# Performance work log

Measured on AMD Instinct MI355X. Metric: run time of the kernel, lower is better.

The kernel has to match this reference:

```python
import jax, jax.numpy as jnp
import numpy as np

D_MODEL = 1024
N_HEADS = 16
D_K = D_MODEL // N_HEADS
RANK = 16
LORA_SCALING = 32.0 / RANK  # alpha / rank = 2.0
LN_EPS = 1e-5


def _lora_linear(x, w, b, A, B):
    # torch nn.Linear: x @ w.T + b ; LoRA: (x @ A @ B) * scaling
    return x @ w.T + b + (x @ A @ B) * LORA_SCALING


def setup_inputs() -> dict:
    key = jax.random.key(0)
    ks = jax.random.split(key, 20)
    d = {}
    d['x'] = jax.random.normal(ks[0], (4, 1024, D_MODEL), dtype=jnp.float32)
    i = 1
    for p in ('q', 'k', 'v', 'o'):
        d[f'{p}_w'] = jax.random.normal(ks[i], (D_MODEL, D_MODEL), dtype=jnp.float32) * (1.0 / np.sqrt(D_MODEL)); i += 1
        d[f'{p}_b'] = jax.random.normal(ks[i], (D_MODEL,), dtype=jnp.float32) * 0.01; i += 1
        d[f'{p}_A'] = jax.random.normal(ks[i], (D_MODEL, RANK), dtype=jnp.float32) * 0.01; i += 1
        d[f'{p}_B'] = jax.random.normal(ks[i], (RANK, D_MODEL), dtype=jnp.float32) * 0.01; i += 1
    d['ln_g'] = jnp.ones((D_MODEL,), dtype=jnp.float32)
    d['ln_b'] = jnp.zeros((D_MODEL,), dtype=jnp.float32)
    return d


def reference(x, q_w, q_b, q_A, q_B, k_w, k_b, k_A, k_B,
              v_w, v_b, v_A, v_B, o_w, o_b, o_A, o_B, ln_g, ln_b):
    B, S, _ = x.shape
    # QKV projections with LoRA, reshape to [B, H, S, d_k]
    def split_heads(t):
        return t.reshape(B, S, N_HEADS, D_K).transpose(0, 2, 1, 3)
    Q = split_heads(_lora_linear(x, q_w, q_b, q_A, q_B))
    K = split_heads(_lora_linear(x, k_w, k_b, k_A, k_B))
    V = split_heads(_lora_linear(x, v_w, v_b, v_A, v_B))

    scores = jnp.einsum('bhqd,bhkd->bhqk', Q, K) / jnp.sqrt(jnp.float32(D_K))
    attn = jax.nn.softmax(scores, axis=-1)  # dropout is identity in eval
    ctx = jnp.einsum('bhqk,bhkd->bhqd', attn, V)
    ctx = ctx.transpose(0, 2, 1, 3).reshape(B, S, D_MODEL)

    out = _lora_linear(ctx, o_w, o_b, o_A, o_B)
    # residual + LayerNorm
    h = out + x
    mu = jnp.mean(h, axis=-1, keepdims=True)
    var = jnp.mean(jnp.square(h - mu), axis=-1, keepdims=True)
    normed = (h - mu) * jax.lax.rsqrt(var + LN_EPS) * ln_g + ln_b
    return normed, attn.mean(axis=1)
```

## Files before the change

kernel.cpp:

```cpp
#include <hip/hip_runtime.h>

#define DMODEL 1024
#define NHEADS 16
#define DHEAD  64
#define RANK   16
#define BATCH  4
#define SEQ    1024
#define MTOT   (BATCH*SEQ)
#define QSCALE 0.18033688011112042f

typedef __bf16 bf16;
typedef __bf16 bf16x8 __attribute__((ext_vector_type(8)));
typedef __bf16 bf16x4 __attribute__((ext_vector_type(4)));
typedef float  f32x4  __attribute__((ext_vector_type(4)));
typedef float  f32x16 __attribute__((ext_vector_type(16)));

__device__ __forceinline__ int swz128(int row, int byte_in_row) {
  int slot = byte_in_row >> 4;
  return row * 128 + (((slot ^ (row & 7)) << 4) | (byte_in_row & 15));
}

__device__ __forceinline__ void gll16(const void* g, void* l) {
  __builtin_amdgcn_global_load_lds((const __attribute__((address_space(1))) unsigned int*)g,
                                   (__attribute__((address_space(3))) unsigned int*)l, 16, 0, 0);
}

__device__ __forceinline__ unsigned pack2(float a, float b) {
  union { bf16 h[2]; unsigned u; } x;
  x.h[0] = (bf16)a; x.h[1] = (bf16)b;
  return x.u;
}

#define PSWAP(a, b) asm volatile("v_permlane32_swap_b32 %0, %1" : "+v"(a), "+v"(b));

__global__ void prep_kernel(
    const float* __restrict__ W0, const float* __restrict__ A0, const float* __restrict__ B0,
    const float* __restrict__ W1, const float* __restrict__ A1, const float* __restrict__ B1,
    const float* __restrict__ W2, const float* __restrict__ A2, const float* __restrict__ B2,
    const float* __restrict__ W3, const float* __restrict__ A3, const float* __restrict__ B3,
    bf16* __restrict__ out, const float* __restrict__ x, bf16* __restrict__ xb) {
  __shared__ float bsc[RANK];
  const int blk = blockIdx.x;
  if (blk < 4096) {
    const int l = blk >> 10;
    const float* W = l == 0 ? W0 : l == 1 ? W1 : l == 2 ? W2 : W3;
    const float* A = l == 0 ? A0 : l == 1 ? A1 : l == 2 ? A2 : A3;
    const float* Bm = l == 0 ? B0 : l == 1 ? B1 : l == 2 ? B2 : B3;
    bf16* o = out + (size_t)l * DMODEL * DMODEL;
    const int n = blk & 1023;
    if (threadIdx.x < RANK) bsc[threadIdx.x] = Bm[threadIdx.x * DMODEL + n] * 2.0f;
    __syncthreads();
    float br[RANK];
#pragma unroll
    for (int r = 0; r < RANK; ++r) br[r] = bsc[r];
    for (int k0 = 0; k0 < DMODEL; k0 += 256) {
      int k = k0 + threadIdx.x;
      float acc = W[n * DMODEL + k];
      const float4* arow = (const float4*)(A + k * RANK);
#pragma unroll
      for (int r4 = 0; r4 < 4; ++r4) {
        float4 a = arow[r4];
        acc += a.x*br[r4*4+0] + a.y*br[r4*4+1] + a.z*br[r4*4+2] + a.w*br[r4*4+3];
      }
      o[n * DMODEL + k] = (bf16)acc;
    }
  } else {
    int i = ((blk - 4096) * 256 + threadIdx.x) * 4;
    float4 v = *(const float4*)(x + i);
    bf16x4 o4 = { (bf16)v.x, (bf16)v.y, (bf16)v.z, (bf16)v.w };
    *(bf16x4*)(xb + i) = o4;
  }
}

__global__ __launch_bounds__(512) void gemm_qkv_kernel(
    const bf16* __restrict__ xb, const bf16* __restrict__ weff,
    const float* __restrict__ bq, const float* __restrict__ bk, const float* __restrict__ bv,
    bf16* __restrict__ Qb, bf16* __restrict__ Kb, bf16* __restrict__ Vt)
{
  __shared__ __align__(16) char sA[16384];
  __shared__ __align__(16) char sB[32768];
  const int tid = threadIdx.x, w = tid >> 6, lane = tid & 63;
  const int bid = blockIdx.x;
  const int nb = (bid & 7) * 48 + (bid >> 3);
  const int n0 = (nb % 12) * 256, m0 = (nb / 12) * 128;
  const int z = n0 >> 10;
  const float* bias = z == 0 ? bq : z == 1 ? bk : bv;
  const float scl = z == 0 ? QSCALE : 1.0f;
  const int wm = (w & 1) * 64, wn = (w >> 1) * 64;
  f32x4 acc[4][4] = {};

  const bf16* pA[2]; const bf16* pB[4]; char* lA[2]; char* lB[4];
#pragma unroll
  for (int i = 0; i < 2; ++i) {
    int ci = i * 8 + w;
    int row = ci * 8 + (lane >> 3);
    int ss = (lane & 7) ^ (row & 7);
    pA[i] = xb + (size_t)(m0 + row) * DMODEL + ss * 8;
    lA[i] = sA + ci * 1024;
  }
#pragma unroll
  for (int i = 0; i < 4; ++i) {
    int ci = i * 8 + w;
    int row = ci * 8 + (lane >> 3);
    int ss = (lane & 7) ^ (row & 7);
    pB[i] = weff + (size_t)(n0 + row) * DMODEL + ss * 8;
    lB[i] = sB + ci * 1024;
  }
  for (int kt = 0; kt < DMODEL / 64; ++kt) {
    const int kbase = kt * 64;
#pragma unroll
    for (int i = 0; i < 2; ++i) gll16(pA[i] + kbase, lA[i]);
#pragma unroll
    for (int i = 0; i < 4; ++i) gll16(pB[i] + kbase, lB[i]);
    __syncthreads();
#pragma unroll
    for (int ks = 0; ks < 2; ++ks) {
      bf16x8 af[4], bfg[4];
#pragma unroll
      for (int mi = 0; mi < 4; ++mi)
        af[mi] = *(const bf16x8*)(sA + swz128(wm + mi*16 + (lane & 15), ks*64 + (lane >> 4)*16));
#pragma unroll
      for (int ni = 0; ni < 4; ++ni)
        bfg[ni] = *(const bf16x8*)(sB + swz128(wn + ni*16 + (lane & 15), ks*64 + (lane >> 4)*16));
#pragma unroll
      for (int mi = 0; mi < 4; ++mi)
#pragma unroll
        for (int ni = 0; ni < 4; ++ni)
          acc[mi][ni] = __builtin_amdgcn_mfma_f32_16x16x32_bf16(af[mi], bfg[ni], acc[mi][ni], 0, 0, 0);
    }
    __syncthreads();
  }

  if (z < 2) {
    bf16* outp = z == 0 ? Qb : Kb;
#pragma unroll
    for (int mi = 0; mi < 4; ++mi) {
#pragma unroll
      for (int ni = 0; ni < 4; ++ni) {
        int col = n0 + wn + ni * 16 + (lane & 15);
        float bcol = bias[col & 1023];
        int h = (col >> 6) & 15, d = col & 63;
#pragma unroll
        for (int r = 0; r < 4; ++r) {
          int row = m0 + wm + mi * 16 + (lane >> 4) * 4 + r;
          float v = (acc[mi][ni][r] + bcol) * scl;
          int b = row >> 10, s = row & 1023;
          outp[(size_t)((b * NHEADS + h) * SEQ + s) * DHEAD + d] = (bf16)v;
        }
      }
    }
  } else {
#pragma unroll
    for (int mi = 0; mi < 4; ++mi) {
#pragma unroll
      for (int ni = 0; ni < 4; ++ni) {
        int col = n0 + wn + ni * 16 + (lane & 15);
        float bcol = bias[col & 1023];
        int h = (col >> 6) & 15, d = col & 63;
        int row0 = m0 + wm + mi * 16 + (lane >> 4) * 4;
        int b = row0 >> 10, s = row0 & 1023;
        bf16x4 pv;
#pragma unroll
        for (int r = 0; r < 4; ++r) pv[r] = (bf16)(acc[mi][ni][r] + bcol);
        *(bf16x4*)(Vt + (size_t)((b * NHEADS + h) * DHEAD + d) * SEQ + s) = pv;
      }
    }
  }
}

__global__ __launch_bounds__(256) void flash_kernel(
    const bf16* __restrict__ Qb, const bf16* __restrict__ Kb, const bf16* __restrict__ Vt,
    bf16* __restrict__ ctx, float* __restrict__ lstat)
{
  __shared__ __align__(16) char sK[2 * 8192];
  __shared__ __align__(16) char sV[2 * 8192];
  const int tid = threadIdx.x, w = tid >> 6, lane = tid & 63;
  const int l31 = lane & 31, lh = lane >> 5;
  const int bid = blockIdx.x;
  const int nb = (bid & 7) * 64 + (bid >> 3);
  const int bh = nb >> 3;
  const int q0 = (nb & 7) * 128;
  const bf16* Qbase = Qb + (size_t)bh * SEQ * DHEAD;
  const bf16* Kbase = Kb + (size_t)bh * SEQ * DHEAD;
  const bf16* Vbase = Vt + (size_t)bh * DHEAD * SEQ;
  const int qw = q0 + w * 32;

  bf16x8 aq[4];
#pragma unroll
  for (int kb = 0; kb < 4; ++kb)
    aq[kb] = *(const bf16x8*)(Qbase + (size_t)(qw + l31) * DHEAD + kb * 16 + lh * 8);

  const bf16* pK[2]; const bf16* pV[2]; int lKo[2], lVo[2];
#pragma unroll
  for (int i = 0; i < 2; ++i) {
    int ci = i * 4 + w;
    int row = ci * 8 + (lane >> 3);
    int ss = (lane & 7) ^ (row & 7);
    pK[i] = Kbase + (size_t)row * DHEAD + ss * 8;
    lKo[i] = ci * 1024;
    pV[i] = Vbase + (size_t)row * SEQ + ss * 8;
    lVo[i] = ci * 1024;
  }

  f32x16 oacc[2] = {};
  float lsum = 0.f;

#pragma unroll
  for (int i = 0; i < 2; ++i) {
    gll16(pK[i], sK + lKo[i]);
    gll16(pV[i], sV + lVo[i]);
  }
  __syncthreads();

  for (int kt = 0; kt < SEQ / 64; ++kt) {
    const int cur = (kt & 1) << 13, nxt = cur ^ 8192;
    if (kt + 1 < SEQ / 64) {
#pragma unroll
      for (int i = 0; i < 2; ++i) {
        gll16(pK[i] + (size_t)(kt + 1) * 64 * DHEAD, sK + nxt + lKo[i]);
        gll16(pV[i] + (kt + 1) * 64, sV + nxt + lVo[i]);
      }
    }

    f32x16 s[2] = {};
    __builtin_amdgcn_s_setprio(1);
#pragma unroll
    for (int ksb = 0; ksb < 2; ++ksb)
#pragma unroll
      for (int kb = 0; kb < 4; ++kb) {
        bf16x8 ak = *(const bf16x8*)(sK + cur + swz128(ksb*32 + l31, kb*32 + lh*16));
        s[ksb] = __builtin_amdgcn_mfma_f32_32x32x16_bf16(ak, aq[kb], s[ksb], 0, 0, 0);
      }
    __builtin_amdgcn_s_setprio(0);

    bf16x8 paf[4];
#pragma unroll
    for (int ksb = 0; ksb < 2; ++ksb) {
      float p[16];
#pragma unroll
      for (int r = 0; r < 16; ++r) {
        p[r] = __builtin_amdgcn_exp2f(s[ksb][r]);
        lsum += p[r];
      }
      unsigned a0 = pack2(p[0], p[1]),   b0 = pack2(p[4], p[5]);
      unsigned a1 = pack2(p[2], p[3]),   b1 = pack2(p[6], p[7]);
      PSWAP(a0, b0) PSWAP(a1, b1)
      unsigned c0 = pack2(p[8], p[9]),   d0 = pack2(p[12], p[13]);
      unsigned c1 = pack2(p[10], p[11]), d1 = pack2(p[14], p[15]);
      PSWAP(c0, d0) PSWAP(c1, d1)
      union { unsigned u[4]; bf16x8 v; } A0, A1;
      A0.u[0] = a0; A0.u[1] = a1; A0.u[2] = b0; A0.u[3] = b1;
      A1.u[0] = c0; A1.u[1] = c1; A1.u[2] = d0; A1.u[3] = d1;
      paf[ksb * 2 + 0] = A0.v;
      paf[ksb * 2 + 1] = A1.v;
    }

    __builtin_amdgcn_s_setprio(1);
#pragma unroll
    for (int kbg = 0; kbg < 4; ++kbg)
#pragma unroll
      for (int db = 0; db < 2; ++db) {
        bf16x8 bv = *(const bf16x8*)(sV + cur + swz128(db*32 + l31, kbg*32 + lh*16));
        oacc[db] = __builtin_amdgcn_mfma_f32_32x32x16_bf16(paf[kbg], bv, oacc[db], 0, 0, 0);
      }
    __builtin_amdgcn_s_setprio(0);

    __syncthreads();
  }

  lsum += __shfl_xor(lsum, 32);
  float inv = __builtin_amdgcn_rcpf(lsum);

  const int b = bh >> 4, hh = bh & 15;
#pragma unroll
  for (int r = 0; r < 16; ++r) {
    int q_r = (r & 3) + 8 * (r >> 2) + 4 * lh;
    float sc = __shfl(inv, q_r);
    int row = qw + q_r;
#pragma unroll
    for (int db = 0; db < 2; ++db)
      ctx[(size_t)(b * SEQ + row) * DMODEL + hh * DHEAD + db * 32 + l31] =
          (bf16)(oacc[db][r] * sc);
  }
  if (lane < 32) lstat[(size_t)bh * SEQ + qw + lane] = lsum;
}

__global__ __launch_bounds__(256) void tail_kernel(
    const bf16* __restrict__ Qb, const bf16* __restrict__ Kb,
    const float* __restrict__ lstat, float* __restrict__ out2,
    const bf16* __restrict__ ctx, const bf16* __restrict__ weffo,
    const float* __restrict__ bias, const float* __restrict__ resid,
    float* __restrict__ outf)
{
  __shared__ __align__(16) char smem[2 * 16384];
  const int tid = threadIdx.x, w = tid >> 6, lane = tid & 63;

  if (blockIdx.x < 512) {
    char* sK = smem;
    const int bid = blockIdx.x;
    const int nb2 = (bid & 7) * 64 + (bid >> 3);
    const int b = nb2 >> 7;
    const int q0 = ((nb2 >> 3) & 15) * 64, k0 = (nb2 & 7) * 128;
    const int qw = q0 + w * 16;
    size_t goff[4]; int lofs[4];
#pragma unroll
    for (int i = 0; i < 4; ++i) {
      int chunk = i * 4 + w;
      int row = chunk * 8 + (lane >> 3);
      int ss = (lane & 7) ^ (row & 7);
      goff[i] = (size_t)(k0 + row) * DHEAD + ss * 8;
      lofs[i] = chunk * 1024;
    }
    const bf16* Kb_b = Kb + (size_t)b * NHEADS * SEQ * DHEAD;
    const bf16* Qb_b = Qb + (size_t)b * NHEADS * SEQ * DHEAD;

    f32x4 macc[8] = {};
#pragma unroll
    for (int i = 0; i < 4; ++i) gll16(Kb_b + goff[i], sK + lofs[i]);
    asm volatile("s_waitcnt vmcnt(0)" ::: "memory");
    __syncthreads();

    for (int h = 0; h < NHEADS; ++h) {
      const int cur = (h & 1) << 14, nxt = cur ^ 16384;
      if (h + 1 < NHEADS) {
        const bf16* Kn = Kb_b + (size_t)(h + 1) * SEQ * DHEAD;
#pragma unroll
        for (int i = 0; i < 4; ++i) gll16(Kn + goff[i], sK + nxt + lofs[i]);
      }
      const bf16* Qbase = Qb_b + (size_t)h * SEQ * DHEAD;
      bf16x8 aq[2];
#pragma unroll
      for (int ks = 0; ks < 2; ++ks)
        aq[ks] = *(const bf16x8*)(Qbase + (size_t)(qw + (lane & 15)) * DHEAD
                                  + ks * 32 + (lane >> 4) * 8);
      char* cK = sK + cur;
      f32x4 sc[8] = {};
#pragma unroll
      for (int ks = 0; ks < 2; ++ks)
#pragma unroll
        for (int ni = 0; ni < 8; ++ni) {
          bf16x8 bk = *(const bf16x8*)(cK + swz128(ni*16 + (lane & 15), ks*64 + (lane >> 4)*16));
          sc[ni] = __builtin_amdgcn_mfma_f32_16x16x32_bf16(aq[ks], bk, sc[ni], 0, 0, 0);
        }
      float lsc[4];
      const float* ls = lstat + ((size_t)(b * NHEADS + h)) * SEQ;
#pragma unroll
      for (int r = 0; r < 4; ++r)
        lsc[r] = 0.0625f * __builtin_amdgcn_rcpf(ls[qw + (lane >> 4)*4 + r]);
#pragma unroll
      for (int ni = 0; ni < 8; ++ni)
#pragma unroll
        for (int r = 0; r < 4; ++r)
          macc[ni][r] += __builtin_amdgcn_exp2f(sc[ni][r]) * lsc[r];
      asm volatile("s_waitcnt vmcnt(0)" ::: "memory");
      __syncthreads();
    }
#pragma unroll
    for (int r = 0; r < 4; ++r) {
      int qrow = qw + (lane >> 4) * 4 + r;
#pragma unroll
      for (int ni = 0; ni < 8; ++ni)
        out2[(size_t)(b * SEQ + qrow) * SEQ + k0 + ni * 16 + (lane & 15)] = macc[ni][r];
    }
  } else {
    char* sA = smem; char* sB = smem + 8192;
    const int bid = blockIdx.x - 512;
    const int nb = (bid & 7) * 64 + (bid >> 3);
    const int n0 = (nb & 7) * 128, m0 = (nb >> 3) * 64;
    const int wm = (w & 1) * 32, wn = (w >> 1) * 64;
    f32x4 acc[2][4] = {};
    const bf16* pA[2]; char* lA[2];
    const bf16* pB[4]; char* lB[4];
#pragma unroll
    for (int i = 0; i < 2; ++i) {
      int chunk = i * 4 + w;
      int row = chunk * 8 + (lane >> 3);
      int ss = (lane & 7) ^ (row & 7);
      pA[i] = ctx + (size_t)(m0 + row) * DMODEL + ss * 8;
      lA[i] = sA + chunk * 1024;
    }
#pragma unroll
    for (int i = 0; i < 4; ++i) {
      int chunk = i * 4 + w;
      int row = chunk * 8 + (lane >> 3);
      int ss = (lane & 7) ^ (row & 7);
      pB[i] = weffo + (size_t)(n0 + row) * DMODEL + ss * 8;
      lB[i] = sB + chunk * 1024;
    }
    for (int kt = 0; kt < DMODEL / 64; ++kt) {
      const int kbase = kt * 64;
#pragma unroll
      for (int i = 0; i < 2; ++i) gll16(pA[i] + kbase, lA[i]);
#pragma unroll
      for (int i = 0; i < 4; ++i) gll16(pB[i] + kbase, lB[i]);
      __syncthreads();
#pragma unroll
      for (int ks = 0; ks < 2; ++ks) {
        bf16x8 af[2], bfg[4];
#pragma unroll
        for (int mi = 0; mi < 2; ++mi)
          af[mi] = *(const bf16x8*)(sA + swz128(wm + mi*16 + (lane & 15), ks*64 + (lane >> 4)*16));
#pragma unroll
        for (int ni = 0; ni < 4; ++ni)
          bfg[ni] = *(const bf16x8*)(sB + swz128(wn + ni*16 + (lane & 15), ks*64 + (lane >> 4)*16));
#pragma unroll
        for (int mi = 0; mi < 2; ++mi)
#pragma unroll
          for (int ni = 0; ni < 4; ++ni)
            acc[mi][ni] = __builtin_amdgcn_mfma_f32_16x16x32_bf16(af[mi], bfg[ni], acc[mi][ni], 0, 0, 0);
      }
      __syncthreads();
    }
#pragma unroll
    for (int mi = 0; mi < 2; ++mi) {
#pragma unroll
      for (int ni = 0; ni < 4; ++ni) {
        int col = n0 + wn + ni * 16 + (lane & 15);
        float bcol = bias[col];
#pragma unroll
        for (int r = 0; r < 4; ++r) {
          int row = m0 + wm + mi * 16 + (lane >> 4) * 4 + r;
          outf[(size_t)row * DMODEL + col] =
              acc[mi][ni][r] + bcol + resid[(size_t)row * DMODEL + col];
        }
      }
    }
  }
}

__global__ __launch_bounds__(256) void ln_kernel(
    float* __restrict__ hb, const float* __restrict__ g,
    const float* __restrict__ bvec, float* __restrict__ out)
{
  const int row = blockIdx.x, t = threadIdx.x;
  float4 v = *(const float4*)(hb + (size_t)row * DMODEL + t * 4);
  float s = v.x + v.y + v.z + v.w;
  float s2 = v.x*v.x + v.y*v.y + v.z*v.z + v.w*v.w;
#pragma unroll
  for (int off = 32; off >= 1; off >>= 1) {
    s  += __shfl_down(s, off);
    s2 += __shfl_down(s2, off);
  }
  __shared__ float red[8];
  const int w = t >> 6;
  if ((t & 63) == 0) { red[w] = s; red[4 + w] = s2; }
  __syncthreads();
  if (t == 0) {
    red[0] = red[0] + red[1] + red[2] + red[3];
    red[4] = red[4] + red[5] + red[6] + red[7];
  }
  __syncthreads();
  float mu = red[0] * (1.0f / DMODEL);
  float var = red[4] * (1.0f / DMODEL) - mu * mu;
  float rs = rsqrtf(var + 1e-5f);
  float4 gv = *(const float4*)(g + t * 4);
  float4 bv = *(const float4*)(bvec + t * 4);
  float4 o;
  o.x = (v.x - mu) * rs * gv.x + bv.x;
  o.y = (v.y - mu) * rs * gv.y + bv.y;
  o.z = (v.z - mu) * rs * gv.z + bv.z;
  o.w = (v.w - mu) * rs * gv.w + bv.w;
  *(float4*)(out + (size_t)row * DMODEL + t * 4) = o;
}

extern "C" void kernel_launch(void* const* d_in, const int* in_sizes, int n_in,
                              void* d_out, int out_size, void* d_ws, size_t ws_size,
                              hipStream_t stream) {
  (void)in_sizes; (void)n_in; (void)out_size; (void)ws_size;
  const float* x = (const float*)d_in[0];
  const float* w_[4]  = {(const float*)d_in[1],  (const float*)d_in[5],
                         (const float*)d_in[9],  (const float*)d_in[13]};
  const float* b_[4]  = {(const float*)d_in[2],  (const float*)d_in[6],
                         (const float*)d_in[10], (const float*)d_in[14]};
  const float* A_[4]  = {(const float*)d_in[3],  (const float*)d_in[7],
                         (const float*)d_in[11], (const float*)d_in[15]};
  const float* Bm_[4] = {(const float*)d_in[4],  (const float*)d_in[8],
                         (const float*)d_in[12], (const float*)d_in[16]};
  const float* lng = (const float*)d_in[17];
  const float* lnb = (const float*)d_in[18];

  char* ws = (char*)d_ws;
  bf16* xb    = (bf16*)(ws);
  bf16* weff  = (bf16*)(ws + (8u  << 20));
  bf16* Qb    = (bf16*)(ws + (16u << 20));
  bf16* Kb    = (bf16*)(ws + (24u << 20));
  bf16* Vt    = (bf16*)(ws + (32u << 20));
  float* lstat = (float*)(ws + (40u << 20));
  bf16* ctx = xb;
  float* hbuf = (float*)d_out;
  float* out2 = (float*)d_out + (size_t)MTOT * DMODEL;

  prep_kernel<<<dim3(8192), dim3(256), 0, stream>>>(
      w_[0], A_[0], Bm_[0], w_[1], A_[1], Bm_[1],
      w_[2], A_[2], Bm_[2], w_[3], A_[3], Bm_[3], weff, x, xb);

  gemm_qkv_kernel<<<dim3(384), 512, 0, stream>>>(
      xb, weff, b_[0], b_[1], b_[2], Qb, Kb, Vt);

  flash_kernel<<<dim3(512), 256, 0, stream>>>(Qb, Kb, Vt, ctx, lstat);

  tail_kernel<<<dim3(1024), 256, 0, stream>>>(
      Qb, Kb, lstat, out2,
      ctx, weff + 3u * DMODEL * DMODEL, b_[3], x, hbuf);

  ln_kernel<<<dim3(MTOT), 256, 0, stream>>>(hbuf, lng, lnb, hbuf);
}
```

Before: 124.4 us.

## Store V in row-major layout and read it with LDS transpose loads

The QKV GEMM now writes V in the same [b,h,s,d] layout as Q and K instead of a transposed V^T layout, which removes the strided transposed-store epilogue. The flash kernel loads V tiles with a custom global-to-LDS address mapping and uses ds_read_b64_tr_b16 transpose reads to build the MFMA B operand. V reads are issued early, overlapping with the softmax, and a full lgkmcnt wait plus a sched barrier precede the PV MFMAs. The risk is that the hand-derived lane/offset mapping is wrong, and that the explicit wait serializes the pipeline.

```diff
diff --git a/kernel.cpp b/kernel.cpp
--- a/kernel.cpp
+++ b/kernel.cpp
@@ -32,6 +32,11 @@
 }
 
 #define PSWAP(a, b) asm volatile("v_permlane32_swap_b32 %0, %1" : "+v"(a), "+v"(b));
+
+#define TRRD(lo, hi, base, o0, o1)                                   \
+  asm volatile("ds_read_b64_tr_b16 %0, %2 offset:" #o0 "\n\t"        \
+               "ds_read_b64_tr_b16 %1, %2 offset:" #o1               \
+               : "=v"(lo), "=v"(hi) : "v"(base));
 
 __global__ void prep_kernel(
     const float* __restrict__ W0, const float* __restrict__ A0, const float* __restrict__ B0,
@@ -75,7 +80,7 @@
 __global__ __launch_bounds__(512) void gemm_qkv_kernel(
     const bf16* __restrict__ xb, const bf16* __restrict__ weff,
     const float* __restrict__ bq, const float* __restrict__ bk, const float* __restrict__ bv,
-    bf16* __restrict__ Qb, bf16* __restrict__ Kb, bf16* __restrict__ Vt)
+    bf16* __restrict__ Qb, bf16* __restrict__ Kb, bf16* __restrict__ Vb)
 {
   __shared__ __align__(16) char sA[16384];
   __shared__ __align__(16) char sB[32768];
@@ -85,6 +90,7 @@
   const int n0 = (nb % 12) * 256, m0 = (nb / 12) * 128;
   const int z = n0 >> 10;
   const float* bias = z == 0 ? bq : z == 1 ? bk : bv;
+  bf16* outp = z == 0 ? Qb : (z == 1 ? Kb : Vb);
   const float scl = z == 0 ? QSCALE : 1.0f;
   const int wm = (w & 1) * 64, wn = (w >> 1) * 64;
   f32x4 acc[4][4] = {};
@@ -131,45 +137,26 @@
     __syncthreads();
   }
 
-  if (z < 2) {
-    bf16* outp = z == 0 ? Qb : Kb;
-#pragma unroll
-    for (int mi = 0; mi < 4; ++mi) {
-#pragma unroll
-      for (int ni = 0; ni < 4; ++ni) {
-        int col = n0 + wn + ni * 16 + (lane & 15);
-        float bcol = bias[col & 1023];
-        int h = (col >> 6) & 15, d = col & 63;
-#pragma unroll
-        for (int r = 0; r < 4; ++r) {
-          int row = m0 + wm + mi * 16 + (lane >> 4) * 4 + r;
-          float v = (acc[mi][ni][r] + bcol) * scl;
-          int b = row >> 10, s = row & 1023;
-          outp[(size_t)((b * NHEADS + h) * SEQ + s) * DHEAD + d] = (bf16)v;
-        }
-      }
-    }
-  } else {
-#pragma unroll
-    for (int mi = 0; mi < 4; ++mi) {
-#pragma unroll
-      for (int ni = 0; ni < 4; ++ni) {
-        int col = n0 + wn + ni * 16 + (lane & 15);
-        float bcol = bias[col & 1023];
-        int h = (col >> 6) & 15, d = col & 63;
-        int row0 = m0 + wm + mi * 16 + (lane >> 4) * 4;
-        int b = row0 >> 10, s = row0 & 1023;
-        bf16x4 pv;
-#pragma unroll
-        for (int r = 0; r < 4; ++r) pv[r] = (bf16)(acc[mi][ni][r] + bcol);
-        *(bf16x4*)(Vt + (size_t)((b * NHEADS + h) * DHEAD + d) * SEQ + s) = pv;
+#pragma unroll
+  for (int mi = 0; mi < 4; ++mi) {
+#pragma unroll
+    for (int ni = 0; ni < 4; ++ni) {
+      int col = n0 + wn + ni * 16 + (lane & 15);
+      float bcol = bias[col & 1023];
+      int h = (col >> 6) & 15, d = col & 63;
+#pragma unroll
+      for (int r = 0; r < 4; ++r) {
+        int row = m0 + wm + mi * 16 + (lane >> 4) * 4 + r;
+        float v = (acc[mi][ni][r] + bcol) * scl;
+        int b = row >> 10, s = row & 1023;
+        outp[(size_t)((b * NHEADS + h) * SEQ + s) * DHEAD + d] = (bf16)v;
       }
     }
   }
 }
 
 __global__ __launch_bounds__(256) void flash_kernel(
-    const bf16* __restrict__ Qb, const bf16* __restrict__ Kb, const bf16* __restrict__ Vt,
+    const bf16* __restrict__ Qb, const bf16* __restrict__ Kb, const bf16* __restrict__ Vb,
     bf16* __restrict__ ctx, float* __restrict__ lstat)
 {
   __shared__ __align__(16) char sK[2 * 8192];
@@ -182,7 +169,7 @@
   const int q0 = (nb & 7) * 128;
   const bf16* Qbase = Qb + (size_t)bh * SEQ * DHEAD;
   const bf16* Kbase = Kb + (size_t)bh * SEQ * DHEAD;
-  const bf16* Vbase = Vt + (size_t)bh * DHEAD * SEQ;
+  const bf16* Vbase = Vb + (size_t)bh * SEQ * DHEAD;
   const int qw = q0 + w * 32;
 
   bf16x8 aq[4];
@@ -194,13 +181,18 @@
 #pragma unroll
   for (int i = 0; i < 2; ++i) {
     int ci = i * 4 + w;
-    int row = ci * 8 + (lane >> 3);
-    int ss = (lane & 7) ^ (row & 7);
-    pK[i] = Kbase + (size_t)row * DHEAD + ss * 8;
+    int rowK = ci * 8 + (lane >> 3);
+    int ssK = (lane & 7) ^ (rowK & 7);
+    pK[i] = Kbase + (size_t)rowK * DHEAD + ssK * 8;
     lKo[i] = ci * 1024;
-    pV[i] = Vbase + (size_t)row * SEQ + ss * 8;
+    int kV = ci * 8 + ((lane >> 5) & 1) * 4 + ((lane >> 1) & 3);
+    int dV = (((lane >> 3) & 3) << 4) + ((lane & 1) << 3);
+    pV[i] = Vbase + (size_t)kV * DHEAD + dV;
     lVo[i] = ci * 1024;
   }
+
+  const unsigned vb0 = (unsigned)(uintptr_t)sV + lh * 1024 + ((lane >> 4) & 1) * 128
+                       + (lane & 15) * 8;
 
   f32x16 oacc[2] = {};
   float lsum = 0.f;
@@ -215,10 +207,11 @@
   for (int kt = 0; kt < SEQ / 64; ++kt) {
     const int cur = (kt & 1) << 13, nxt = cur ^ 8192;
     if (kt + 1 < SEQ / 64) {
+      const size_t kofs = (size_t)(kt + 1) * 64 * DHEAD;
 #pragma unroll
       for (int i = 0; i < 2; ++i) {
-        gll16(pK[i] + (size_t)(kt + 1) * 64 * DHEAD, sK + nxt + lKo[i]);
-        gll16(pV[i] + (kt + 1) * 64, sV + nxt + lVo[i]);
+        gll16(pK[i] + kofs, sK + nxt + lKo[i]);
+        gll16(pV[i] + kofs, sV + nxt + lVo[i]);
       }
     }
 
@@ -232,6 +225,17 @@
         s[ksb] = __builtin_amdgcn_mfma_f32_32x32x16_bf16(ak, aq[kb], s[ksb], 0, 0, 0);
       }
     __builtin_amdgcn_s_setprio(0);
+
+    unsigned long long v0[4][2], v1[4][2];
+    const unsigned vb = vb0 + cur;
+    TRRD(v0[0][0], v1[0][0], vb, 0, 512)
+    TRRD(v0[0][1], v1[0][1], vb, 256, 768)
+    TRRD(v0[1][0], v1[1][0], vb, 2048, 2560)
+    TRRD(v0[1][1], v1[1][1], vb, 2304, 2816)
+    TRRD(v0[2][0], v1[2][0], vb, 4096, 4608)
+    TRRD(v0[2][1], v1[2][1], vb, 4352, 4864)
+    TRRD(v0[3][0], v1[3][0], vb, 6144, 6656)
+    TRRD(v0[3][1], v1[3][1], vb, 6400, 6912)
 
     bf16x8 paf[4];
 #pragma unroll
@@ -255,13 +259,17 @@
       paf[ksb * 2 + 1] = A1.v;
     }
 
+    asm volatile("s_waitcnt lgkmcnt(0)" ::: "memory");
+    __builtin_amdgcn_sched_barrier(0);
+
     __builtin_amdgcn_s_setprio(1);
 #pragma unroll
     for (int kbg = 0; kbg < 4; ++kbg)
 #pragma unroll
       for (int db = 0; db < 2; ++db) {
-        bf16x8 bv = *(const bf16x8*)(sV + cur + swz128(db*32 + l31, kbg*32 + lh*16));
-        oacc[db] = __builtin_amdgcn_mfma_f32_32x32x16_bf16(paf[kbg], bv, oacc[db], 0, 0, 0);
+        union { unsigned long long u[2]; bf16x8 v; } V;
+        V.u[0] = v0[kbg][db]; V.u[1] = v1[kbg][db];
+        oacc[db] = __builtin_amdgcn_mfma_f32_32x32x16_bf16(paf[kbg], V.v, oacc[db], 0, 0, 0);
       }
     __builtin_amdgcn_s_setprio(0);
 
@@ -484,7 +492,7 @@
   bf16* weff  = (bf16*)(ws + (8u  << 20));
   bf16* Qb    = (bf16*)(ws + (16u << 20));
   bf16* Kb    = (bf16*)(ws + (24u << 20));
-  bf16* Vt    = (bf16*)(ws + (32u << 20));
+  bf16* Vb    = (bf16*)(ws + (32u << 20));
   float* lstat = (float*)(ws + (40u << 20));
   bf16* ctx = xb;
   float* hbuf = (float*)d_out;
@@ -495,9 +503,9 @@
       w_[2], A_[2], Bm_[2], w_[3], A_[3], Bm_[3], weff, x, xb);
 
   gemm_qkv_kernel<<<dim3(384), 512, 0, stream>>>(
-      xb, weff, b_[0], b_[1], b_[2], Qb, Kb, Vt);
-
-  flash_kernel<<<dim3(512), 256, 0, stream>>>(Qb, Kb, Vt, ctx, lstat);
+      xb, weff, b_[0], b_[1], b_[2], Qb, Kb, Vb);
+
+  flash_kernel<<<dim3(512), 256, 0, stream>>>(Qb, Kb, Vb, ctx, lstat);
 
   tail_kernel<<<dim3(1024), 256, 0, stream>>>(
       Qb, Kb, lstat, out2,
```

Measured after the change: 122.9 us. Within noise of the previous version (-1.2%).
